# Kernel optimization log

Measured on AMD Instinct MI355X. Metric: run time of the kernel, lower is better.

## Reference

```python
import jax, jax.numpy as jnp
import numpy as np

N_EMBD = 768
N_HEAD = 8
HEAD_DIM = N_EMBD // N_HEAD


def setup_inputs() -> dict:
    key = jax.random.key(0)
    k1, k2, k3, k4, k5 = jax.random.split(key, 5)
    B, T, C = 8, 1024, N_EMBD
    scale = 0.02
    return {
        "x": jax.random.normal(k1, (B, T, C), dtype=jnp.float32),
        "W_attn": jax.random.normal(k2, (C, 3 * C), dtype=jnp.float32) * scale,
        "b_attn": jnp.zeros((3 * C,), dtype=jnp.float32),
        "W_proj": jax.random.normal(k3, (C, C), dtype=jnp.float32) * scale,
        "b_proj": jnp.zeros((C,), dtype=jnp.float32),
    }


def reference(x, W_attn, b_attn, W_proj, b_proj):
    B, T, C = x.shape
    H, D = N_HEAD, HEAD_DIM
    qkv = x @ W_attn + b_attn                      # [B,T,3C]
    q, k, v = jnp.split(qkv, 3, axis=-1)
    # [B,H,T,D]
    q = q.reshape(B, T, H, D).transpose(0, 2, 1, 3)
    k = k.reshape(B, T, H, D).transpose(0, 2, 1, 3)
    v = v.reshape(B, T, H, D).transpose(0, 2, 1, 3)
    att = jnp.einsum("bhqd,bhkd->bhqk", q, k) * (1.0 / jnp.sqrt(jnp.float32(D)))
    causal = jnp.tril(jnp.ones((T, T), dtype=bool))
    att = jnp.where(causal[None, None], att, jnp.float32(-jnp.inf))
    att = jax.nn.softmax(att, axis=-1)
    y = jnp.einsum("bhqk,bhkd->bhqd", att, v)      # [B,H,T,D]
    y = y.transpose(0, 2, 1, 3).reshape(B, T, C)
    return y @ W_proj + b_proj
```

## Files before the change

### kernel.cpp

```cpp
#include <hip/hip_runtime.h>
#include <math.h>

#define B_ 8
#define T_ 1024
#define C_ 768
#define H_ 8
#define D_ 96
#define M_ (B_ * T_)
#define N1_ (3 * C_)
#define KD_ 768

typedef __bf16 bf16x8 __attribute__((ext_vector_type(8)));
typedef float f32x4 __attribute__((ext_vector_type(4)));
typedef float f32x16 __attribute__((ext_vector_type(16)));

__device__ __forceinline__ unsigned short f2bf(float f) {
  unsigned int u = __float_as_uint(f);
  u += 0x7FFF + ((u >> 16) & 1);
  return (unsigned short)(u >> 16);
}

__device__ __forceinline__ void load_lds16(const void* g, void* l) {
  __builtin_amdgcn_global_load_lds(
      (const __attribute__((address_space(1))) unsigned int*)g,
      (__attribute__((address_space(3))) unsigned int*)l, 16, 0, 0);
}

__global__ __launch_bounds__(256) void prep_kernel(
    const float* __restrict__ x, unsigned short* __restrict__ xb,
    const float* __restrict__ Wa, unsigned short* __restrict__ WaT,
    const float* __restrict__ Wp, unsigned short* __restrict__ WpT) {
  __shared__ float Lt[32][33];
  int bid = blockIdx.x;
  if (bid < 6144) {
    int i = (bid * 256 + threadIdx.x) * 4;
    float4 v = *(const float4*)(x + i);
    ushort4 o;
    o.x = f2bf(v.x); o.y = f2bf(v.y); o.z = f2bf(v.z); o.w = f2bf(v.w);
    *(ushort4*)(xb + i) = o;
    return;
  }
  bid -= 6144;
  const float* W; unsigned short* WT; int Nd;
  if (bid < 1728) { W = Wa; WT = WaT; Nd = N1_; }
  else            { W = Wp; WT = WpT; Nd = C_; bid -= 1728; }
  const int r0 = (bid % 24) * 32;
  const int c0 = (bid / 24) * 32;
#pragma unroll
  for (int i = 0; i < 4; ++i) {
    int e = threadIdx.x + 256 * i;
    int r = e >> 5, c = e & 31;
    Lt[r][c] = W[(size_t)(r0 + r) * Nd + c0 + c];
  }
  __syncthreads();
#pragma unroll
  for (int i = 0; i < 4; ++i) {
    int e = threadIdx.x + 256 * i;
    int rr = e >> 5, cc = e & 31;
    WT[(size_t)(c0 + rr) * KD_ + r0 + cc] = f2bf(Lt[cc][rr]);
  }
}

template <int WM32, bool OUTF32, bool VSCAT>
__global__ __launch_bounds__(256, WM32 == 2 ? 3 : 4) void gemm_mfma_kernel(
    const unsigned short* __restrict__ A, const unsigned short* __restrict__ Bt,
    const float* __restrict__ bias, void* __restrict__ Cout,
    unsigned short* __restrict__ vt, int N,
    int sc_lim, float sc, int mmask, int mshift) {
  constexpr int AS2 = 2 * WM32;
  constexpr int NCH = AS2 * 2 + 8;
  constexpr int CPW = NCH / 4;
  __shared__ __align__(16) unsigned short Sb[3][NCH * 512];
  const int tid = threadIdx.x;
  const int w = tid >> 6, l = tid & 63;
  const int l31 = l & 31, lh = l >> 5;
  const int bid = blockIdx.x;
  const int m0 = (bid & mmask) * (AS2 * 32), n0 = (bid >> mshift) * 128;
  const int wrb = (w >> 1) * WM32;
  const int wnb = (w & 1) * 2;

  f32x16 acc[WM32][2];
#pragma unroll
  for (int i = 0; i < WM32; ++i)
#pragma unroll
    for (int j = 0; j < 2; ++j)
#pragma unroll
      for (int r = 0; r < 16; ++r) acc[i][j][r] = 0.f;

  const unsigned short* gp[CPW];
#pragma unroll
  for (int i = 0; i < CPW; ++i) {
    const int c = w * CPW + i;
    const int pr = c >> 1, kh = c & 1;
    gp[i] = (pr < AS2)
        ? A  + (size_t)(m0 + pr * 32 + l31) * KD_ + kh * 16 + lh * 8
        : Bt + (size_t)(n0 + (pr - AS2) * 32 + l31) * KD_ + kh * 16 + lh * 8;
  }

#pragma unroll
  for (int t = 0; t < 2; ++t)
#pragma unroll
    for (int i = 0; i < CPW; ++i) {
      load_lds16(gp[i], &Sb[t][(w * CPW + i) * 512]);
      gp[i] += 32;
    }

  int cur = 0, stg = 2;
  for (int k0 = 0; k0 < KD_; k0 += 32) {
    if (k0 + 32 < KD_) {
      if constexpr (CPW == 4) asm volatile("s_waitcnt vmcnt(4)" ::: "memory");
      else                    asm volatile("s_waitcnt vmcnt(3)" ::: "memory");
    } else {
      asm volatile("s_waitcnt vmcnt(0)" ::: "memory");
    }
    __builtin_amdgcn_s_barrier();
    asm volatile("" ::: "memory");

    if (k0 + 64 < KD_) {
#pragma unroll
      for (int i = 0; i < CPW; ++i) {
        load_lds16(gp[i], &Sb[stg][(w * CPW + i) * 512]);
        gp[i] += 32;
      }
    }

#pragma unroll
    for (int kh = 0; kh < 2; ++kh) {
      bf16x8 af[WM32], bfr[2];
#pragma unroll
      for (int mi = 0; mi < WM32; ++mi)
        af[mi] = *(const bf16x8*)&Sb[cur][((wrb + mi) * 2 + kh) * 512 + l * 8];
#pragma unroll
      for (int ni = 0; ni < 2; ++ni)
        bfr[ni] = *(const bf16x8*)&Sb[cur][((AS2 + wnb + ni) * 2 + kh) * 512 + l * 8];
#pragma unroll
      for (int mi = 0; mi < WM32; ++mi)
#pragma unroll
        for (int ni = 0; ni < 2; ++ni)
          acc[mi][ni] = __builtin_amdgcn_mfma_f32_32x32x16_bf16(
              af[mi], bfr[ni], acc[mi][ni], 0, 0, 0);
    }
    cur = (cur == 2) ? 0 : cur + 1;
    stg = (stg == 2) ? 0 : stg + 1;
  }

  const bool vblock = VSCAT && (n0 >= 1536);
#pragma unroll
  for (int mi = 0; mi < WM32; ++mi) {
    const int rowb = m0 + (wrb + mi) * 32 + 4 * lh;
#pragma unroll
    for (int ni = 0; ni < 2; ++ni) {
      const int col = n0 + (wnb + ni) * 32 + l31;
      const float bv = bias[col];
      if (!vblock) {
        const float mul = (col < sc_lim) ? sc : 1.f;
#pragma unroll
        for (int r = 0; r < 16; ++r) {
          const int row = rowb + (r & 3) + 8 * (r >> 2);
          float v = (acc[mi][ni][r] + bv) * mul;
          if (OUTF32)
            ((float*)Cout)[(size_t)row * N + col] = v;
          else
            ((unsigned short*)Cout)[(size_t)row * N + col] = f2bf(v);
        }
      } else {
        const int x = col - 1536;
        const int h = x / 96, d = x % 96;
#pragma unroll
        for (int r = 0; r < 16; ++r) {
          const int row = rowb + (r & 3) + 8 * (r >> 2);
          const int bb = row >> 10, t = row & 1023;
          vt[((size_t)(bb * H_ + h) * D_ + d) * T_ + t] =
              f2bf(acc[mi][ni][r] + bv);
        }
      }
    }
  }
}

__global__ __launch_bounds__(256) void attn_mfma_kernel(
    const unsigned short* __restrict__ qkv,
    const unsigned short* __restrict__ vt,
    unsigned short* __restrict__ y) {
  __shared__ __align__(16) unsigned short KV[2][24 * 512];
  __shared__ __align__(16) unsigned short Pt[4][16][72];

  const int tid = threadIdx.x;
  const int w = tid >> 6, l = tid & 63;
  const int lm = l & 15, lq = l >> 4;
  const int bh = blockIdx.x & 63, pi = blockIdx.x >> 6;
  const int b = bh >> 3, h = bh & 7;
  const size_t bT = (size_t)b * T_;

  bf16x8 onef;
#pragma unroll
  for (int i = 0; i < 8; ++i) onef[i] = (__bf16)1.0f;

  auto issue = [&](int j0, int buf) {
#pragma unroll
    for (int i = 0; i < 6; ++i) {
      const int c = w * 6 + i;
      const unsigned short* g;
      if (c < 12) {
        const int kc = c >> 2, nb = c & 3;
        g = qkv + (bT + j0 + nb * 16 + lm) * N1_ + C_ + h * D_ + kc * 32 + lq * 8;
      } else {
        const int cv = c - 12;
        const int db = cv >> 1, vc = cv & 1;
        g = vt + ((size_t)bh * D_ + db * 16 + lm) * T_ + j0 + vc * 32 + lq * 8;
      }
      load_lds16(g, &KV[buf][c * 512]);
    }
  };

  int cur = 0;
  issue(0, 0);

  for (int half = 0; half < 2; ++half) {
    const int qt = half ? (15 - pi) : pi;
    const int q0 = qt * 64;

    bf16x8 qf[3];
    {
      const unsigned short* qp =
          qkv + (bT + q0 + w * 16 + lm) * N1_ + h * D_ + lq * 8;
      qf[0] = *(const bf16x8*)(qp);
      qf[1] = *(const bf16x8*)(qp + 32);
      qf[2] = *(const bf16x8*)(qp + 64);
    }
    f32x4 o[7];
#pragma unroll
    for (int i = 0; i < 7; ++i) o[i] = (f32x4){0.f, 0.f, 0.f, 0.f};

    for (int jt = 0; jt <= qt; ++jt) {
      __syncthreads();
      if (jt < qt)          issue((jt + 1) * 64, cur ^ 1);
      else if (half == 0)   issue(0, cur ^ 1);

      const bool diag = (jt == qt);
#pragma unroll
      for (int nb = 0; nb < 4; ++nb) {
        if (diag && nb > w) {
#pragma unroll
          for (int r = 0; r < 4; ++r)
            Pt[w][lq * 4 + r][nb * 16 + lm] = 0;
          continue;
        }
        f32x4 a = (f32x4){0.f, 0.f, 0.f, 0.f};
#pragma unroll
        for (int kc = 0; kc < 3; ++kc) {
          bf16x8 kf = *(const bf16x8*)&KV[cur][(kc * 4 + nb) * 512 + l * 8];
          a = __builtin_amdgcn_mfma_f32_16x16x32_bf16(qf[kc], kf, a, 0, 0, 0);
        }
#pragma unroll
        for (int r = 0; r < 4; ++r) {
          float s = a[r];
          if (diag && (nb * 16 + lm > w * 16 + lq * 4 + r)) s = -INFINITY;
          Pt[w][lq * 4 + r][nb * 16 + lm] = f2bf(__expf(s));
        }
      }

      bf16x8 pf0 = *(const bf16x8*)&Pt[w][lm][lq * 8];
      bf16x8 pf1 = *(const bf16x8*)&Pt[w][lm][32 + lq * 8];
#pragma unroll
      for (int db = 0; db < 6; ++db) {
        bf16x8 vf0 = *(const bf16x8*)&KV[cur][(12 + db * 2 + 0) * 512 + l * 8];
        bf16x8 vf1 = *(const bf16x8*)&KV[cur][(12 + db * 2 + 1) * 512 + l * 8];
        o[db] = __builtin_amdgcn_mfma_f32_16x16x32_bf16(pf0, vf0, o[db], 0, 0, 0);
        o[db] = __builtin_amdgcn_mfma_f32_16x16x32_bf16(pf1, vf1, o[db], 0, 0, 0);
      }
      o[6] = __builtin_amdgcn_mfma_f32_16x16x32_bf16(pf0, onef, o[6], 0, 0, 0);
      o[6] = __builtin_amdgcn_mfma_f32_16x16x32_bf16(pf1, onef, o[6], 0, 0, 0);
      cur ^= 1;
    }

#pragma unroll
    for (int r = 0; r < 4; ++r) {
      const float inv = 1.f / o[6][r];
      const size_t row = bT + q0 + w * 16 + lq * 4 + r;
#pragma unroll
      for (int db = 0; db < 6; ++db)
        y[row * C_ + h * D_ + db * 16 + lm] = f2bf(o[db][r] * inv);
    }
  }
}

extern "C" void kernel_launch(void* const* d_in, const int* in_sizes, int n_in,
                              void* d_out, int out_size, void* d_ws, size_t ws_size,
                              hipStream_t stream) {
  const float* x      = (const float*)d_in[0];
  const float* W_attn = (const float*)d_in[1];
  const float* b_attn = (const float*)d_in[2];
  const float* W_proj = (const float*)d_in[3];
  const float* b_proj = (const float*)d_in[4];
  float* out = (float*)d_out;

  char* ws = (char*)d_ws;
  unsigned short* xb  = (unsigned short*)(ws);
  unsigned short* WaT = (unsigned short*)(ws + 12582912);
  unsigned short* WpT = (unsigned short*)(ws + 16121856);
  unsigned short* qkv = (unsigned short*)(ws + 17301504);
  unsigned short* vt  = (unsigned short*)(ws + 55050240);
  unsigned short* yb  = (unsigned short*)(ws + 67633152);

  const float qscale = 0.10206207261596577f;

  prep_kernel<<<6144 + 2304, 256, 0, stream>>>(x, xb, W_attn, WaT, W_proj, WpT);

  gemm_mfma_kernel<2, false, true><<<(N1_ / 128) * (M_ / 128), 256, 0, stream>>>(
      xb, WaT, b_attn, qkv, vt, N1_, C_, qscale, 63, 6);
  attn_mfma_kernel<<<8 * B_ * H_, 256, 0, stream>>>(qkv, vt, yb);
  gemm_mfma_kernel<1, true, false><<<(C_ / 128) * (M_ / 64), 256, 0, stream>>>(
      yb, WpT, b_proj, out, nullptr, C_, 0, 1.f, 127, 7);
}
```

Baseline: 216.9 us.

## Add 256x256-tile QKV GEMM kernel with 4-stage LDS pipeline

Replaces the QKV projection GEMM with a new kernel that uses 512 threads and 256x256 output tiles. It runs a 4-buffer global-to-LDS prefetch pipeline with explicit vmcnt waits, uses a swizzled block order for L2 locality, and raises MFMA priority with setprio. The larger tile is meant to increase operand reuse and cut global/LDS traffic per FLOP. In exchange it uses more registers and LDS per block (128KB shared, occupancy 2), launches fewer blocks (288), and the epilogue writes to qkv and vt with scattered stores.

```diff
diff --git a/kernel.cpp b/kernel.cpp
--- a/kernel.cpp
+++ b/kernel.cpp
@@ -58,6 +58,108 @@
     int e = threadIdx.x + 256 * i;
     int rr = e >> 5, cc = e & 31;
     WT[(size_t)(c0 + rr) * KD_ + r0 + cc] = f2bf(Lt[cc][rr]);
+  }
+}
+
+__global__ __launch_bounds__(512, 2) void gemm256_kernel(
+    const unsigned short* __restrict__ A, const unsigned short* __restrict__ Bt,
+    const float* __restrict__ bias, unsigned short* __restrict__ Cout,
+    unsigned short* __restrict__ vt, float sc) {
+  __shared__ __align__(16) unsigned short Sb[4][32 * 512];
+  const int tid = threadIdx.x;
+  const int w = tid >> 6, l = tid & 63;
+  const int l31 = l & 31, lh = l >> 5;
+  const int wm = w >> 2, wn = w & 3;
+
+  const int bid = blockIdx.x;
+  const int swz = (bid & 7) * 36 + (bid >> 3);
+  const int m0 = (swz & 31) * 256, n0 = (swz >> 5) * 256;
+
+  f32x16 acc[4][2];
+#pragma unroll
+  for (int mi = 0; mi < 4; ++mi)
+#pragma unroll
+    for (int ni = 0; ni < 2; ++ni)
+#pragma unroll
+      for (int r = 0; r < 16; ++r) acc[mi][ni][r] = 0.f;
+
+  const unsigned short* gp[4];
+#pragma unroll
+  for (int i = 0; i < 4; ++i) {
+    const int c = w * 4 + i;
+    const int kh = c & 1, pr = (c >> 1) & 7;
+    gp[i] = (c < 16)
+        ? A  + (size_t)(m0 + pr * 32 + l31) * KD_ + kh * 16 + lh * 8
+        : Bt + (size_t)(n0 + pr * 32 + l31) * KD_ + kh * 16 + lh * 8;
+  }
+
+  auto stage = [&](int buf) {
+#pragma unroll
+    for (int i = 0; i < 4; ++i) {
+      load_lds16(gp[i], &Sb[buf][(w * 4 + i) * 512]);
+      gp[i] += 32;
+    }
+  };
+
+  stage(0); stage(1); stage(2);
+
+  for (int t = 0; t < 24; ++t) {
+    const int ahead = 23 - t;
+    if (ahead >= 2)      asm volatile("s_waitcnt vmcnt(8)" ::: "memory");
+    else if (ahead == 1) asm volatile("s_waitcnt vmcnt(4)" ::: "memory");
+    else                 asm volatile("s_waitcnt vmcnt(0)" ::: "memory");
+    __builtin_amdgcn_s_barrier();
+    asm volatile("" ::: "memory");
+
+    if (t + 3 < 24) stage((t + 3) & 3);
+
+    const int cb = t & 3;
+#pragma unroll
+    for (int kh = 0; kh < 2; ++kh) {
+      bf16x8 af[4], bfr[2];
+#pragma unroll
+      for (int mi = 0; mi < 4; ++mi)
+        af[mi] = *(const bf16x8*)&Sb[cb][((wm * 4 + mi) * 2 + kh) * 512 + l * 8];
+#pragma unroll
+      for (int ni = 0; ni < 2; ++ni)
+        bfr[ni] = *(const bf16x8*)&Sb[cb][(16 + (wn * 2 + ni) * 2 + kh) * 512 + l * 8];
+      __builtin_amdgcn_s_setprio(1);
+#pragma unroll
+      for (int mi = 0; mi < 4; ++mi)
+#pragma unroll
+        for (int ni = 0; ni < 2; ++ni)
+          acc[mi][ni] = __builtin_amdgcn_mfma_f32_32x32x16_bf16(
+              af[mi], bfr[ni], acc[mi][ni], 0, 0, 0);
+      __builtin_amdgcn_s_setprio(0);
+    }
+  }
+
+#pragma unroll
+  for (int mi = 0; mi < 4; ++mi) {
+    const int rowb = m0 + wm * 128 + mi * 32 + 4 * lh;
+#pragma unroll
+    for (int ni = 0; ni < 2; ++ni) {
+      const int col = n0 + wn * 64 + ni * 32 + l31;
+      const float bv = bias[col];
+      if (col < 1536) {
+        const float mul = (col < C_) ? sc : 1.f;
+#pragma unroll
+        for (int r = 0; r < 16; ++r) {
+          const int row = rowb + (r & 3) + 8 * (r >> 2);
+          Cout[(size_t)row * N1_ + col] = f2bf((acc[mi][ni][r] + bv) * mul);
+        }
+      } else {
+        const int x = col - 1536;
+        const int h = x / 96, d = x % 96;
+#pragma unroll
+        for (int r = 0; r < 16; ++r) {
+          const int row = rowb + (r & 3) + 8 * (r >> 2);
+          const int bb = row >> 10, t = row & 1023;
+          vt[((size_t)(bb * H_ + h) * D_ + d) * T_ + t] =
+              f2bf(acc[mi][ni][r] + bv);
+        }
+      }
+    }
   }
 }
 
@@ -307,8 +409,8 @@
 
   prep_kernel<<<6144 + 2304, 256, 0, stream>>>(x, xb, W_attn, WaT, W_proj, WpT);
 
-  gemm_mfma_kernel<2, false, true><<<(N1_ / 128) * (M_ / 128), 256, 0, stream>>>(
-      xb, WaT, b_attn, qkv, vt, N1_, C_, qscale, 63, 6);
+  gemm256_kernel<<<(M_ / 256) * (N1_ / 256), 512, 0, stream>>>(
+      xb, WaT, b_attn, qkv, vt, qscale);
   attn_mfma_kernel<<<8 * B_ * H_, 256, 0, stream>>>(qkv, vt, yb);
   gemm_mfma_kernel<1, true, false><<<(C_ / 128) * (M_ / 64), 256, 0, stream>>>(
       yb, WpT, b_proj, out, nullptr, C_, 0, 1.f, 127, 7);
```

After: 233.6 us. +7.7%, slower.

## Swizzle GEMM LDS layout and use 128x128 tiles for projection GEMM

Applied to the files above, without the earlier changes.

Rewrites how the GEMM kernel lays out A/B tiles in LDS. Each 64-byte row chunk is now loaded as 16-row groups with an XOR swizzle on the 16-byte column index, and the fragment reads use the same swizzle, to avoid LDS bank conflicts. The template parameter WM32 is removed, so the output projection GEMM now also uses 128x128 tiles, which halves its block count. Launch bounds become 4 waves per SIMD for both GEMMs, which may constrain registers for the QKV GEMM.

```diff
diff --git a/kernel.cpp b/kernel.cpp
--- a/kernel.cpp
+++ b/kernel.cpp
@@ -61,27 +61,26 @@
   }
 }
 
-template <int WM32, bool OUTF32, bool VSCAT>
-__global__ __launch_bounds__(256, WM32 == 2 ? 3 : 4) void gemm_mfma_kernel(
+template <bool OUTF32, bool VSCAT>
+__global__ __launch_bounds__(256, 4) void gemm_mfma_kernel(
     const unsigned short* __restrict__ A, const unsigned short* __restrict__ Bt,
     const float* __restrict__ bias, void* __restrict__ Cout,
     unsigned short* __restrict__ vt, int N,
     int sc_lim, float sc, int mmask, int mshift) {
-  constexpr int AS2 = 2 * WM32;
-  constexpr int NCH = AS2 * 2 + 8;
-  constexpr int CPW = NCH / 4;
+  constexpr int NCH = 16;
+  constexpr int CPW = 4;
   __shared__ __align__(16) unsigned short Sb[3][NCH * 512];
   const int tid = threadIdx.x;
   const int w = tid >> 6, l = tid & 63;
   const int l31 = l & 31, lh = l >> 5;
   const int bid = blockIdx.x;
-  const int m0 = (bid & mmask) * (AS2 * 32), n0 = (bid >> mshift) * 128;
-  const int wrb = (w >> 1) * WM32;
+  const int m0 = (bid & mmask) * 128, n0 = (bid >> mshift) * 128;
+  const int wrb = (w >> 1) * 2;
   const int wnb = (w & 1) * 2;
 
-  f32x16 acc[WM32][2];
-#pragma unroll
-  for (int i = 0; i < WM32; ++i)
+  f32x16 acc[2][2];
+#pragma unroll
+  for (int i = 0; i < 2; ++i)
 #pragma unroll
     for (int j = 0; j < 2; ++j)
 #pragma unroll
@@ -91,10 +90,10 @@
 #pragma unroll
   for (int i = 0; i < CPW; ++i) {
     const int c = w * CPW + i;
-    const int pr = c >> 1, kh = c & 1;
-    gp[i] = (pr < AS2)
-        ? A  + (size_t)(m0 + pr * 32 + l31) * KD_ + kh * 16 + lh * 8
-        : Bt + (size_t)(n0 + (pr - AS2) * 32 + l31) * KD_ + kh * 16 + lh * 8;
+    const int rr = (c & 7) * 16 + (l >> 2);
+    const int ck = 8 * ((l & 3) ^ ((l >> 2) & 3));
+    gp[i] = (c < 8) ? A  + (size_t)(m0 + rr) * KD_ + ck
+                    : Bt + (size_t)(n0 + rr) * KD_ + ck;
   }
 
 #pragma unroll
@@ -105,11 +104,14 @@
       gp[i] += 32;
     }
 
+  const int rhi = l31 >> 4;
+  const int rlo = (l31 & 15) * 32;
+  const int rx  = l31 & 3;
+
   int cur = 0, stg = 2;
   for (int k0 = 0; k0 < KD_; k0 += 32) {
     if (k0 + 32 < KD_) {
-      if constexpr (CPW == 4) asm volatile("s_waitcnt vmcnt(4)" ::: "memory");
-      else                    asm volatile("s_waitcnt vmcnt(3)" ::: "memory");
+      asm volatile("s_waitcnt vmcnt(4)" ::: "memory");
     } else {
       asm volatile("s_waitcnt vmcnt(0)" ::: "memory");
     }
@@ -126,15 +128,18 @@
 
 #pragma unroll
     for (int kh = 0; kh < 2; ++kh) {
-      bf16x8 af[WM32], bfr[2];
-#pragma unroll
-      for (int mi = 0; mi < WM32; ++mi)
-        af[mi] = *(const bf16x8*)&Sb[cur][((wrb + mi) * 2 + kh) * 512 + l * 8];
+      const int q = 2 * kh + lh;
+      bf16x8 af[2], bfr[2];
+#pragma unroll
+      for (int mi = 0; mi < 2; ++mi)
+        af[mi] = *(const bf16x8*)
+            &Sb[cur][((wrb + mi) * 2 + rhi) * 512 + rlo + ((q ^ rx)) * 8];
 #pragma unroll
       for (int ni = 0; ni < 2; ++ni)
-        bfr[ni] = *(const bf16x8*)&Sb[cur][((AS2 + wnb + ni) * 2 + kh) * 512 + l * 8];
-#pragma unroll
-      for (int mi = 0; mi < WM32; ++mi)
+        bfr[ni] = *(const bf16x8*)
+            &Sb[cur][(8 + (wnb + ni) * 2 + rhi) * 512 + rlo + ((q ^ rx)) * 8];
+#pragma unroll
+      for (int mi = 0; mi < 2; ++mi)
 #pragma unroll
         for (int ni = 0; ni < 2; ++ni)
           acc[mi][ni] = __builtin_amdgcn_mfma_f32_32x32x16_bf16(
@@ -146,7 +151,7 @@
 
   const bool vblock = VSCAT && (n0 >= 1536);
 #pragma unroll
-  for (int mi = 0; mi < WM32; ++mi) {
+  for (int mi = 0; mi < 2; ++mi) {
     const int rowb = m0 + (wrb + mi) * 32 + 4 * lh;
 #pragma unroll
     for (int ni = 0; ni < 2; ++ni) {
@@ -307,9 +312,9 @@
 
   prep_kernel<<<6144 + 2304, 256, 0, stream>>>(x, xb, W_attn, WaT, W_proj, WpT);
 
-  gemm_mfma_kernel<2, false, true><<<(N1_ / 128) * (M_ / 128), 256, 0, stream>>>(
+  gemm_mfma_kernel<false, true><<<(N1_ / 128) * (M_ / 128), 256, 0, stream>>>(
       xb, WaT, b_attn, qkv, vt, N1_, C_, qscale, 63, 6);
   attn_mfma_kernel<<<8 * B_ * H_, 256, 0, stream>>>(qkv, vt, yb);
-  gemm_mfma_kernel<1, true, false><<<(C_ / 128) * (M_ / 64), 256, 0, stream>>>(
-      yb, WpT, b_proj, out, nullptr, C_, 0, 1.f, 127, 7);
-}
+  gemm_mfma_kernel<true, false><<<(C_ / 128) * (M_ / 128), 256, 0, stream>>>(
+      yb, WpT, b_proj, out, nullptr, C_, 0, 1.f, 63, 6);
+}
```

Result: faster. 193.0 us (-11.0%).
